# Kernel tuning notes

Measured on AMD Instinct MI355X. Metric: run time of the kernel, lower is better.

## Reference

```python
import jax, jax.numpy as jnp
import numpy as np

B, S, E, H, DK, DV = 2, 2048, 1024, 16, 64, 64
NEG = -1e9


def setup_inputs() -> dict:
    key = jax.random.key(0)
    ks = jax.random.split(key, 12)
    s = 0.02
    return {
        "query": jax.random.normal(ks[0], (B, S, E), jnp.float32),
        "key": jax.random.normal(ks[1], (B, S, E), jnp.float32),
        "value": jax.random.normal(ks[2], (B, S, E), jnp.float32),
        "mask": jax.random.randint(ks[3], (B, S, S), 0, 2, jnp.int32),
        "Wq": jax.random.normal(ks[4], (E, H * DK), jnp.float32) * s,
        "bq": jnp.zeros((H * DK,), jnp.float32),
        "Wk": jax.random.normal(ks[5], (E, H * DK), jnp.float32) * s,
        "bk": jnp.zeros((H * DK,), jnp.float32),
        "Wv": jax.random.normal(ks[6], (E, H * DV), jnp.float32) * s,
        "bv": jnp.zeros((H * DV,), jnp.float32),
        "Wo": jax.random.normal(ks[7], (H * DV, E), jnp.float32) * s,
        "bo": jnp.zeros((E,), jnp.float32),
    }


def reference(query, key, value, mask, Wq, bq, Wk, bk, Wv, bv, Wo, bo):
    # projections, then split heads: (B,S,H*D) -> (B,H,S,D)
    q = (query @ Wq + bq).reshape(B, S, H, DK).transpose(0, 2, 1, 3)
    k = (key @ Wk + bk).reshape(B, S, H, DK).transpose(0, 2, 1, 3)
    v = (value @ Wv + bv).reshape(B, S, H, DV).transpose(0, 2, 1, 3)
    scores = jnp.einsum("bhqd,bhkd->bhqk", q, k) / jnp.sqrt(jnp.float32(DK))
    scores = jnp.where(mask[:, None, :, :] == 0, jnp.float32(NEG), scores)
    weights = jax.nn.softmax(scores, axis=-1)
    ctx = jnp.einsum("bhqk,bhkd->bhqd", weights, v)
    ctx = ctx.transpose(0, 2, 1, 3).reshape(B, S, H * DV)
    return ctx @ Wo + bo
```

## Files before the change

kernel.cpp:

```cpp
#include <hip/hip_runtime.h>

typedef __attribute__((ext_vector_type(8))) short s16x8;
typedef __attribute__((ext_vector_type(4))) float f32x4;
typedef unsigned short u16;
typedef unsigned int u32;
typedef unsigned long long u64;

__device__ __forceinline__ u16 f2bf(float f) {
  u32 u = __builtin_bit_cast(u32, f);
  u += 0x7fff + ((u >> 16) & 1);
  return (u16)(u >> 16);
}

__device__ __forceinline__ float exp2fast(float x) {
#if __has_builtin(__builtin_amdgcn_exp2f)
  return __builtin_amdgcn_exp2f(x);
#else
  return __expf(x * 0.6931471805599453f);
#endif
}

__device__ __forceinline__ void gload16(const void* g, void* l) {
  __builtin_amdgcn_global_load_lds((const __attribute__((address_space(1))) u32*)g,
                                   (__attribute__((address_space(3))) u32*)l, 16, 0, 0);
}

#define MFMA(a, b, c) __builtin_amdgcn_mfma_f32_16x16x32_bf16((a), (b), (c), 0, 0, 0)

#define QSCALE 0.18033688011112042f

__global__ __launch_bounds__(256) void cvt_bf16_3(const float* __restrict__ q,
                                                  const float* __restrict__ k,
                                                  const float* __restrict__ v,
                                                  u16* __restrict__ oq, u16* __restrict__ ok,
                                                  u16* __restrict__ ov) {
  int z = blockIdx.y;
  const float* src = (z == 0) ? q : (z == 1) ? k : v;
  u16* dst = (z == 0) ? oq : (z == 1) ? ok : ov;
  int i = blockIdx.x * 256 + threadIdx.x;
  const float4* s4 = (const float4*)src;
  float4 a = s4[2 * i], b = s4[2 * i + 1];
  uint4 o;
  o.x = (u32)f2bf(a.x) | ((u32)f2bf(a.y) << 16);
  o.y = (u32)f2bf(a.z) | ((u32)f2bf(a.w) << 16);
  o.z = (u32)f2bf(b.x) | ((u32)f2bf(b.y) << 16);
  o.w = (u32)f2bf(b.z) | ((u32)f2bf(b.w) << 16);
  ((uint4*)dst)[i] = o;
}

__global__ __launch_bounds__(256) void mask_bits(const int* __restrict__ mask,
                                                 u64* __restrict__ mb) {
  int wi = (blockIdx.x * 256 + threadIdx.x) >> 6;
  int lane = threadIdx.x & 63;
  u64 bits = __ballot(mask[((size_t)wi << 6) + lane] != 0);
  if (lane == 0) mb[wi] = bits;
}

__global__ __launch_bounds__(256) void transpose_w4(const float* __restrict__ W0,
                                                    const float* __restrict__ W1,
                                                    const float* __restrict__ W2,
                                                    const float* __restrict__ W3,
                                                    u16* __restrict__ T0, u16* __restrict__ T1,
                                                    u16* __restrict__ T2, u16* __restrict__ T3) {
  int z = blockIdx.z;
  const float* W = (z == 0) ? W0 : (z == 1) ? W1 : (z == 2) ? W2 : W3;
  u16* WT = (z == 0) ? T0 : (z == 1) ? T1 : (z == 2) ? T2 : T3;
  __shared__ float t[32][33];
  int tx = threadIdx.x, ty = threadIdx.y;
  int n = blockIdx.x * 32 + tx;
#pragma unroll
  for (int j = 0; j < 4; j++) {
    int k = blockIdx.y * 32 + ty + 8 * j;
    t[ty + 8 * j][tx] = W[(size_t)k * 1024 + n];
  }
  __syncthreads();
  int k = blockIdx.y * 32 + tx;
#pragma unroll
  for (int j = 0; j < 4; j++) {
    int n2 = blockIdx.x * 32 + ty + 8 * j;
    WT[(size_t)n2 * 1024 + k] = f2bf(t[tx][ty + 8 * j]);
  }
}

template <int BM, int BN>
__device__ __forceinline__ void gemm_core(const u16* __restrict__ A, const u16* __restrict__ BT,
                                          int m0, int n0, u16* Ash, u16* Bsh,
                                          f32x4 (&acc)[BM / 32][BN / 32]) {
  constexpr int MF = BM / 32, NF = BN / 32;
  const int tid = threadIdx.x;
  const int lane = tid & 63, wid = tid >> 6;
  const int r16 = lane & 15, g = lane >> 4;
  const int wm = wid >> 1, wn = wid & 1;
  const f32x4 vz = {0.f, 0.f, 0.f, 0.f};
#pragma unroll
  for (int mf = 0; mf < MF; mf++)
#pragma unroll
    for (int nf = 0; nf < NF; nf++) acc[mf][nf] = vz;

  for (int k0 = 0; k0 < 1024; k0 += 64) {
#pragma unroll
    for (int i = 0; i < BM / 32; i++) {
      int ch = i * 256 + tid;
      gload16((const char*)A + (((size_t)(m0 + (ch >> 3)) << 10) + k0 + ((ch & 7) << 3)) * 2,
              (char*)Ash + ch * 16);
    }
#pragma unroll
    for (int i = 0; i < BN / 32; i++) {
      int ch = i * 256 + tid;
      gload16((const char*)BT + (((size_t)(n0 + (ch >> 3)) << 10) + k0 + ((ch & 7) << 3)) * 2,
              (char*)Bsh + ch * 16);
    }
    __syncthreads();
#pragma unroll
    for (int kk = 0; kk < 2; kk++) {
      s16x8 af[MF], bfr[NF];
#pragma unroll
      for (int mf = 0; mf < MF; mf++)
        af[mf] = *(const s16x8*)(Ash + ((wm * (BM / 2) + mf * 16 + r16) << 6) + kk * 32 + g * 8);
#pragma unroll
      for (int nf = 0; nf < NF; nf++)
        bfr[nf] = *(const s16x8*)(Bsh + ((wn * (BN / 2) + nf * 16 + r16) << 6) + kk * 32 + g * 8);
#pragma unroll
      for (int mf = 0; mf < MF; mf++)
#pragma unroll
        for (int nf = 0; nf < NF; nf++) acc[mf][nf] = MFMA(af[mf], bfr[nf], acc[mf][nf]);
    }
    __syncthreads();
  }
}

__global__ __launch_bounds__(256) void proj_gemm(
    const u16* __restrict__ Xq, const u16* __restrict__ Xk, const u16* __restrict__ Xv,
    const u16* __restrict__ WqT, const u16* __restrict__ WkT, const u16* __restrict__ WvT,
    const float* __restrict__ bq, const float* __restrict__ bk, const float* __restrict__ bv,
    u16* __restrict__ Qo, u16* __restrict__ Ko, u16* __restrict__ Vto) {
  __shared__ u16 Ash[128 * 64], Bsh[128 * 64];
  const int z = blockIdx.z;
  const u16* A = (z == 0) ? Xq : (z == 1) ? Xk : Xv;
  const u16* BT = (z == 0) ? WqT : (z == 1) ? WkT : WvT;
  const float* bias = (z == 0) ? bq : (z == 1) ? bk : bv;
  u16* O = (z == 0) ? Qo : (z == 1) ? Ko : Vto;
  const float sc = (z == 0) ? QSCALE : 1.0f;
  const int m0 = blockIdx.y * 128, n0 = blockIdx.x * 128;
  f32x4 acc[4][4];
  gemm_core<128, 128>(A, BT, m0, n0, Ash, Bsh, acc);
  const int tid = threadIdx.x, lane = tid & 63, wid = tid >> 6;
  const int r16 = lane & 15, g = lane >> 4, wm = wid >> 1, wn = wid & 1;
#pragma unroll
  for (int nf = 0; nf < 4; nf++) {
    int col = n0 + wn * 64 + nf * 16 + r16;
    float bb = bias[col];
    int h = col >> 6, d = col & 63;
#pragma unroll
    for (int mf = 0; mf < 4; mf++) {
#pragma unroll
      for (int ri = 0; ri < 4; ri++) {
        int row = m0 + wm * 64 + mf * 16 + g * 4 + ri;
        int b_ = row >> 11, s_ = row & 2047;
        u16 val = f2bf((acc[mf][nf][ri] + bb) * sc);
        if (z < 2)
          O[((((size_t)b_ * 16 + h) * 2048 + s_) << 6) + d] = val;
        else
          O[((((size_t)b_ * 16 + h) * 64 + d) << 11) + s_] = val;
      }
    }
  }
}

__global__ __launch_bounds__(256) void out_gemm(const u16* __restrict__ ctx,
                                                const u16* __restrict__ WoT,
                                                const float* __restrict__ bo,
                                                float* __restrict__ out) {
  __shared__ u16 Ash[64 * 64], Bsh[128 * 64];
  const int m0 = blockIdx.y * 64, n0 = blockIdx.x * 128;
  f32x4 acc[2][4];
  gemm_core<64, 128>(ctx, WoT, m0, n0, Ash, Bsh, acc);
  const int tid = threadIdx.x, lane = tid & 63, wid = tid >> 6;
  const int r16 = lane & 15, g = lane >> 4, wm = wid >> 1, wn = wid & 1;
#pragma unroll
  for (int nf = 0; nf < 4; nf++) {
    int col = n0 + wn * 64 + nf * 16 + r16;
    float bb = bo[col];
#pragma unroll
    for (int mf = 0; mf < 2; mf++) {
#pragma unroll
      for (int ri = 0; ri < 4; ri++) {
        int row = m0 + wm * 32 + mf * 16 + g * 4 + ri;
        out[((size_t)row << 10) + col] = acc[mf][nf][ri] + bb;
      }
    }
  }
}

__global__ __launch_bounds__(256, 2) void flash_attn(const u16* __restrict__ Q,
                                                     const u16* __restrict__ K,
                                                     const u16* __restrict__ Vt,
                                                     const u64* __restrict__ Mb64,
                                                     u16* __restrict__ ctx) {
  __shared__ __align__(16) u16 Ksh[2][64][64];
  __shared__ __align__(16) u16 Vsh[2][64][64];
  __shared__ __align__(16) u16 P[4][32][72];

  const int tid = threadIdx.x, w = tid >> 6, lane = tid & 63;
  const int r16 = lane & 15, g = lane >> 4;
  const int b = blockIdx.z, h = blockIdx.y;
  const int q0 = blockIdx.x * 128 + w * 32;
  const u16* Qb = Q + ((size_t)(b * 16 + h) << 17);
  const u16* Kb = K + ((size_t)(b * 16 + h) << 17);
  const u16* Vb = Vt + ((size_t)(b * 16 + h) << 17);
  const u64* Mrow0 = Mb64 + ((size_t)(b * 2048 + q0 + r16) << 5);
  const u64* Mrow1 = Mb64 + ((size_t)(b * 2048 + q0 + 16 + r16) << 5);
  u16* Pw = &P[w][0][0];

  const int srow = tid >> 3, sk16 = tid & 7;
#define STAGE(buf, kv0)                                                                   \
  {                                                                                       \
    _Pragma("unroll") for (int i = 0; i < 2; i++) {                                       \
      int row = i * 32 + srow;                                                            \
      int sc = sk16 ^ (row & 7);                                                          \
      gload16(Kb + (((size_t)((kv0) + row)) << 6) + sc * 8,                               \
              (char*)&Ksh[buf][0][0] + (i * 256 + tid) * 16);                             \
      gload16(Vb + (((size_t)row) << 11) + (kv0) + sc * 8,                                \
              (char*)&Vsh[buf][0][0] + (i * 256 + tid) * 16);                             \
    }                                                                                     \
  }

  s16x8 aq[2][2];
#pragma unroll
  for (int qb = 0; qb < 2; qb++)
#pragma unroll
    for (int c = 0; c < 2; c++)
      aq[qb][c] = *(const s16x8*)(Qb + ((q0 + qb * 16 + r16) << 6) + c * 32 + g * 8);
  asm volatile("" ::: "memory");
  STAGE(0, 0);
  u64 mcur0 = Mrow0[0], mcur1 = Mrow1[0];
  asm volatile("" ::: "memory");
  STAGE(1, 64);
  u64 mnext0 = Mrow0[1], mnext1 = Mrow1[1];
  asm volatile("" ::: "memory");

  s16x8 vones;
#pragma unroll
  for (int j = 0; j < 8; j++) vones[j] = (short)0x3F80;

  const f32x4 vz = {0.f, 0.f, 0.f, 0.f};
  f32x4 o[2][4], o4[2];
#pragma unroll
  for (int qb = 0; qb < 2; qb++) {
    o4[qb] = vz;
#pragma unroll
    for (int i = 0; i < 4; i++) o[qb][i] = vz;
  }

  for (int t = 0; t < 32; t++) {
    const int cur = t & 1;
    if (t == 31) {
      asm volatile("s_waitcnt vmcnt(0)" ::: "memory");
    } else {
      asm volatile("s_waitcnt vmcnt(6)" ::: "memory");
    }
    asm volatile("s_barrier" ::: "memory");

    f32x4 s_[2][4];
#pragma unroll
    for (int qb = 0; qb < 2; qb++)
#pragma unroll
      for (int nt = 0; nt < 4; nt++) s_[qb][nt] = vz;
    __builtin_amdgcn_s_setprio(1);
#pragma unroll
    for (int c = 0; c < 2; c++) {
#pragma unroll
      for (int nt = 0; nt < 4; nt++) {
        s16x8 ak = *(const s16x8*)((char*)&Ksh[cur][0][0] + (nt * 16 + r16) * 128 +
                                   (((c * 4 + g) ^ (r16 & 7)) << 4));
        s_[0][nt] = MFMA(ak, aq[0][c], s_[0][nt]);
        s_[1][nt] = MFMA(ak, aq[1][c], s_[1][nt]);
      }
    }
    __builtin_amdgcn_s_setprio(0);

#pragma unroll
    for (int qb = 0; qb < 2; qb++) {
      u64 m = ((qb == 0) ? mcur0 : mcur1) >> (g * 4);
      u32 mlo = (u32)m, mhi = (u32)(m >> 32);
#pragma unroll
      for (int nt = 0; nt < 4; nt++) {
        u32 word = (nt < 2) ? mlo : mhi;
        u32 sh = (nt & 1) << 4;
        float e0 = exp2fast(s_[qb][nt][0]) * (float)((word >> (sh + 0)) & 1);
        float e1 = exp2fast(s_[qb][nt][1]) * (float)((word >> (sh + 1)) & 1);
        float e2 = exp2fast(s_[qb][nt][2]) * (float)((word >> (sh + 2)) & 1);
        float e3 = exp2fast(s_[qb][nt][3]) * (float)((word >> (sh + 3)) & 1);
        u32 pk0, pk1;
        asm("v_cvt_pk_bf16_f32 %0, %1, %2" : "=v"(pk0) : "v"(e0), "v"(e1));
        asm("v_cvt_pk_bf16_f32 %0, %1, %2" : "=v"(pk1) : "v"(e2), "v"(e3));
        uint2 pr; pr.x = pk0; pr.y = pk1;
        *(uint2*)((char*)Pw + (qb * 16 + r16) * 144 + nt * 32 + g * 8) = pr;
      }
    }
    asm volatile("" ::: "memory");

    __builtin_amdgcn_s_setprio(1);
#pragma unroll
    for (int c = 0; c < 2; c++) {
      s16x8 pa0 = *(const s16x8*)((char*)Pw + r16 * 144 + c * 64 + g * 16);
      s16x8 pa1 = *(const s16x8*)((char*)Pw + (16 + r16) * 144 + c * 64 + g * 16);
#pragma unroll
      for (int nt = 0; nt < 4; nt++) {
        s16x8 bv = *(const s16x8*)((char*)&Vsh[cur][0][0] + (nt * 16 + r16) * 128 +
                                   (((c * 4 + g) ^ (r16 & 7)) << 4));
        o[0][nt] = MFMA(pa0, bv, o[0][nt]);
        o[1][nt] = MFMA(pa1, bv, o[1][nt]);
      }
      o4[0] = MFMA(pa0, vones, o4[0]);
      o4[1] = MFMA(pa1, vones, o4[1]);
    }
    __builtin_amdgcn_s_setprio(0);

    asm volatile("s_barrier" ::: "memory");
    u64 mnew0 = 0, mnew1 = 0;
    if (t + 2 < 32) {
      STAGE(cur, (t + 2) * 64);
      mnew0 = Mrow0[t + 2];
      mnew1 = Mrow1[t + 2];
    }
    mcur0 = mnext0; mcur1 = mnext1;
    mnext0 = mnew0; mnext1 = mnew1;
  }
#undef STAGE

#pragma unroll
  for (int qb = 0; qb < 2; qb++) {
    float invq[4];
#pragma unroll
    for (int ri = 0; ri < 4; ri++) invq[ri] = 1.f / o4[qb][ri];
#pragma unroll
    for (int nt = 0; nt < 4; nt++) {
      int col = (h << 6) + nt * 16 + r16;
#pragma unroll
      for (int ri = 0; ri < 4; ri++) {
        int row = (b << 11) + q0 + qb * 16 + g * 4 + ri;
        ctx[((size_t)row << 10) + col] = f2bf(o[qb][nt][ri] * invq[ri]);
      }
    }
  }
}

extern "C" void kernel_launch(void* const* d_in, const int* in_sizes, int n_in,
                              void* d_out, int out_size, void* d_ws, size_t ws_size,
                              hipStream_t stream) {
  const float* query = (const float*)d_in[0];
  const float* key_  = (const float*)d_in[1];
  const float* value = (const float*)d_in[2];
  const int*   mask  = (const int*)d_in[3];
  const float* Wq = (const float*)d_in[4];
  const float* bq = (const float*)d_in[5];
  const float* Wk = (const float*)d_in[6];
  const float* bk = (const float*)d_in[7];
  const float* Wv = (const float*)d_in[8];
  const float* bv = (const float*)d_in[9];
  const float* Wo = (const float*)d_in[10];
  const float* bo = (const float*)d_in[11];

  const size_t MB = 1048576;
  char* ws = (char*)d_ws;
  u16* Xq  = (u16*)(ws + 0 * MB);
  u16* Xk  = (u16*)(ws + 8 * MB);
  u16* Xv  = (u16*)(ws + 16 * MB);
  u16* WqT = (u16*)(ws + 24 * MB);
  u16* WkT = (u16*)(ws + 26 * MB);
  u16* WvT = (u16*)(ws + 28 * MB);
  u16* WoT = (u16*)(ws + 30 * MB);
  u16* Qd  = (u16*)(ws + 32 * MB);
  u16* Kd  = (u16*)(ws + 40 * MB);
  u16* Vtd = (u16*)(ws + 48 * MB);
  u16* ctx = (u16*)(ws + 56 * MB);
  u64* Mb  = (u64*)(ws + 72 * MB);

  cvt_bf16_3<<<dim3(2048, 3), 256, 0, stream>>>(query, key_, value, Xq, Xk, Xv);
  mask_bits<<<32768, 256, 0, stream>>>(mask, Mb);

  dim3 tb(32, 8);
  transpose_w4<<<dim3(32, 32, 4), tb, 0, stream>>>(Wq, Wk, Wv, Wo, WqT, WkT, WvT, WoT);

  proj_gemm<<<dim3(8, 32, 3), 256, 0, stream>>>(Xq, Xk, Xv, WqT, WkT, WvT, bq, bk, bv,
                                                Qd, Kd, Vtd);
  flash_attn<<<dim3(16, 16, 2), 256, 0, stream>>>(Qd, Kd, Vtd, Mb, ctx);
  out_gemm<<<dim3(8, 64), 256, 0, stream>>>(ctx, WoT, bo, (float*)d_out);
}
```

Before: 176.0 us.

## Double-buffer GEMM LDS tiles with async prefetch and XOR swizzle

Reworks the shared GEMM core used by the projection and output GEMMs. It now keeps two LDS buffers and prefetches the tile two steps ahead, with explicit vmcnt waits and raw barriers in place of the full syncthreads pair. It also XOR-swizzles the 16-byte chunk column by row to avoid LDS bank conflicts on fragment reads, and sets wave priority around the MFMA section. This targets exposed global-load latency and LDS conflicts, but doubles LDS per block and depends on hand-counted vmcnt values being correct.

```diff
diff --git a/kernel.cpp b/kernel.cpp
--- a/kernel.cpp
+++ b/kernel.cpp
@@ -87,54 +87,85 @@
                                           int m0, int n0, u16* Ash, u16* Bsh,
                                           f32x4 (&acc)[BM / 32][BN / 32]) {
   constexpr int MF = BM / 32, NF = BN / 32;
+  constexpr int BATCH = BM / 32 + BN / 32;
   const int tid = threadIdx.x;
   const int lane = tid & 63, wid = tid >> 6;
   const int r16 = lane & 15, g = lane >> 4;
   const int wm = wid >> 1, wn = wid & 1;
+  const int swz = r16 & 7;
   const f32x4 vz = {0.f, 0.f, 0.f, 0.f};
 #pragma unroll
   for (int mf = 0; mf < MF; mf++)
 #pragma unroll
     for (int nf = 0; nf < NF; nf++) acc[mf][nf] = vz;
 
-  for (int k0 = 0; k0 < 1024; k0 += 64) {
-#pragma unroll
-    for (int i = 0; i < BM / 32; i++) {
+  auto stage = [&](int buf, int k0) {
+#pragma unroll
+    for (int i = 0; i < MF; i++) {
       int ch = i * 256 + tid;
-      gload16((const char*)A + (((size_t)(m0 + (ch >> 3)) << 10) + k0 + ((ch & 7) << 3)) * 2,
-              (char*)Ash + ch * 16);
-    }
-#pragma unroll
-    for (int i = 0; i < BN / 32; i++) {
+      int row = ch >> 3, sc = (ch & 7) ^ (row & 7);
+      gload16(A + (((size_t)(m0 + row)) << 10) + k0 + sc * 8,
+              Ash + (size_t)buf * (BM * 64) + ch * 8);
+    }
+#pragma unroll
+    for (int i = 0; i < NF; i++) {
       int ch = i * 256 + tid;
-      gload16((const char*)BT + (((size_t)(n0 + (ch >> 3)) << 10) + k0 + ((ch & 7) << 3)) * 2,
-              (char*)Bsh + ch * 16);
-    }
-    __syncthreads();
+      int row = ch >> 3, sc = (ch & 7) ^ (row & 7);
+      gload16(BT + (((size_t)(n0 + row)) << 10) + k0 + sc * 8,
+              Bsh + (size_t)buf * (BN * 64) + ch * 8);
+    }
+  };
+
+  asm volatile("" ::: "memory");
+  stage(0, 0);
+  asm volatile("" ::: "memory");
+  stage(1, 64);
+  asm volatile("" ::: "memory");
+
+  for (int t = 0; t < 16; t++) {
+    const int cur = t & 1;
+    if (t == 15) {
+      asm volatile("s_waitcnt vmcnt(0)" ::: "memory");
+    } else if constexpr (BATCH == 8) {
+      asm volatile("s_waitcnt vmcnt(8)" ::: "memory");
+    } else {
+      asm volatile("s_waitcnt vmcnt(6)" ::: "memory");
+    }
+    asm volatile("s_barrier" ::: "memory");
+
+    const u16* Acur = Ash + (size_t)cur * (BM * 64);
+    const u16* Bcur = Bsh + (size_t)cur * (BN * 64);
+    __builtin_amdgcn_s_setprio(1);
 #pragma unroll
     for (int kk = 0; kk < 2; kk++) {
+      const int c = (kk * 4 + g);
       s16x8 af[MF], bfr[NF];
 #pragma unroll
       for (int mf = 0; mf < MF; mf++)
-        af[mf] = *(const s16x8*)(Ash + ((wm * (BM / 2) + mf * 16 + r16) << 6) + kk * 32 + g * 8);
+        af[mf] = *(const s16x8*)(Acur + ((wm * (BM / 2) + mf * 16 + r16) << 6) +
+                                 ((c ^ swz) << 3));
 #pragma unroll
       for (int nf = 0; nf < NF; nf++)
-        bfr[nf] = *(const s16x8*)(Bsh + ((wn * (BN / 2) + nf * 16 + r16) << 6) + kk * 32 + g * 8);
+        bfr[nf] = *(const s16x8*)(Bcur + ((wn * (BN / 2) + nf * 16 + r16) << 6) +
+                                  ((c ^ swz) << 3));
 #pragma unroll
       for (int mf = 0; mf < MF; mf++)
 #pragma unroll
         for (int nf = 0; nf < NF; nf++) acc[mf][nf] = MFMA(af[mf], bfr[nf], acc[mf][nf]);
     }
-    __syncthreads();
-  }
-}
-
-__global__ __launch_bounds__(256) void proj_gemm(
+    __builtin_amdgcn_s_setprio(0);
+
+    asm volatile("s_barrier" ::: "memory");
+    if (t + 2 < 16) stage(cur, (t + 2) * 64);
+  }
+}
+
+__global__ __launch_bounds__(256, 2) void proj_gemm(
     const u16* __restrict__ Xq, const u16* __restrict__ Xk, const u16* __restrict__ Xv,
     const u16* __restrict__ WqT, const u16* __restrict__ WkT, const u16* __restrict__ WvT,
     const float* __restrict__ bq, const float* __restrict__ bk, const float* __restrict__ bv,
     u16* __restrict__ Qo, u16* __restrict__ Ko, u16* __restrict__ Vto) {
-  __shared__ u16 Ash[128 * 64], Bsh[128 * 64];
+  __shared__ u16 Ash[2 * 128 * 64], Bsh[2 * 128 * 64];
   const int z = blockIdx.z;
   const u16* A = (z == 0) ? Xq : (z == 1) ? Xk : Xv;
   const u16* BT = (z == 0) ? WqT : (z == 1) ? WkT : WvT;
@@ -167,11 +198,11 @@
   }
 }
 
-__global__ __launch_bounds__(256) void out_gemm(const u16* __restrict__ ctx,
-                                                const u16* __restrict__ WoT,
-                                                const float* __restrict__ bo,
-                                                float* __restrict__ out) {
-  __shared__ u16 Ash[64 * 64], Bsh[128 * 64];
+__global__ __launch_bounds__(256, 2) void out_gemm(const u16* __restrict__ ctx,
+                                                   const u16* __restrict__ WoT,
+                                                   const float* __restrict__ bo,
+                                                   float* __restrict__ out) {
+  __shared__ u16 Ash[2 * 64 * 64], Bsh[2 * 128 * 64];
   const int m0 = blockIdx.y * 64, n0 = blockIdx.x * 128;
   f32x4 acc[2][4];
   gemm_core<64, 128>(ctx, WoT, m0, n0, Ash, Bsh, acc);
```

Result: faster. 159.0 us (-9.7%).
